# Kernel optimization log

Hardware: AMD Instinct MI355X
Metric: run time of the kernel (lower is better)

Reference implementation:

```python
import jax, jax.numpy as jnp
import numpy as np

N_INPUT, N_HIDDEN, N_OUTPUT = 64, 1024, 64
B, T = 128, 512

def setup_inputs() -> dict:
    key = jax.random.key(0)
    ks = jax.random.split(key, 8)
    s_in = 1.0 / np.sqrt(N_INPUT)
    s_h = 1.0 / np.sqrt(N_HIDDEN)
    return {
        "x": jax.random.normal(ks[0], (B, T, N_INPUT), jnp.float32),
        "enc_w": jax.random.uniform(ks[1], (N_HIDDEN, N_INPUT), jnp.float32, -s_in, s_in),
        "enc_b": jax.random.uniform(ks[2], (N_HIDDEN,), jnp.float32, -s_in, s_in),
        "rec_w": jax.random.uniform(ks[3], (N_HIDDEN, N_HIDDEN), jnp.float32, -s_h, s_h),
        "fgt_w": jax.random.uniform(ks[4], (N_HIDDEN, N_HIDDEN), jnp.float32, -s_h, s_h),
        "dec_w": jax.random.uniform(ks[5], (N_OUTPUT, N_HIDDEN), jnp.float32, -s_h, s_h),
        "dec_b": jax.random.uniform(ks[6], (N_OUTPUT,), jnp.float32, -s_h, s_h),
        "hinit_w": jax.random.uniform(ks[7], (N_HIDDEN, 1), jnp.float32, -1.0, 1.0),
        "hinit_b": jax.random.uniform(jax.random.fold_in(key, 9), (N_HIDDEN,), jnp.float32, -1.0, 1.0),
    }

def softsign(x):
    return x / (1.0 + jnp.abs(x))

def reference(x, enc_w, enc_b, rec_w, fgt_w, dec_w, dec_b, hinit_w, hinit_b):
    # x: [B, T, I] -> time-major [T, B, I]
    xt = jnp.transpose(x, (1, 0, 2))
    # hidden_init(ones(B,1)) = ones @ hinit_w^T + b = broadcast of column sum
    hidden0 = jnp.broadcast_to(hinit_w[:, 0] + hinit_b, (x.shape[0], hinit_b.shape[0]))
    # Precompute encoder projection for all timesteps (same math, one big GEMM)
    enc_all = jnp.einsum('tbi,hi->tbh', xt, enc_w) + enc_b  # [T, B, H]

    def step(hidden, enc_t):
        forget = jax.nn.sigmoid(hidden @ fgt_w.T)
        hidden_new = softsign(enc_t + hidden @ rec_w.T)
        hidden = (1.0 - forget) * hidden + forget * hidden_new
        out_t = hidden @ dec_w.T + dec_b
        return hidden, out_t

    hidden, output = jax.lax.scan(step, hidden0, enc_all)
    return output, hidden  # output: [T, B, O], hidden: [B, H]
```

## Files before the change

kernel.cpp:

```cpp
#include <hip/hip_runtime.h>

typedef unsigned short u16;

#define NWG 256
#define NT  256
#define TS  512
#define HD  1024
#define BS  128
#define NI  64
#define NO  64
#define XR  16
#define CC  32
#define RCP 17
#define MBW2 32

typedef __attribute__((ext_vector_type(8))) short bf16x8;
typedef __attribute__((ext_vector_type(4))) float f32x4;

__device__ __forceinline__ float bf2f(u16 u) {
    union { unsigned int i; float f; } v; v.i = ((unsigned int)u) << 16; return v.f;
}
__device__ __forceinline__ u16 f2bf(float f) {
    union { float fl; unsigned int i; } v; v.fl = f;
    unsigned int x = v.i;
    return (u16)((x + 0x7fffu + ((x >> 16) & 1u)) >> 16);
}
__device__ __forceinline__ float ldv(const void* p, size_t i, bool isf32) {
    return isf32 ? ((const float*)p)[i] : bf2f(((const u16*)p)[i]);
}

__device__ __forceinline__ unsigned l2_atomic_add(unsigned* p, unsigned v) {
    unsigned old;
    asm volatile("global_atomic_add %0, %1, %2, off sc0\n\t"
                 "s_waitcnt vmcnt(0)"
                 : "=&v"(old) : "v"(p), "v"(v) : "memory");
    return old;
}
__device__ __forceinline__ void l2_atomic_swap_nr(unsigned* p, unsigned v) {
    asm volatile("global_atomic_swap %0, %1, off" :: "v"(p), "v"(v) : "memory");
}

__device__ __forceinline__ void load_a_frags(const u16* ap, bf16x8* a) {
    asm volatile(
        "global_load_dwordx4 %0, %8, off sc0\n\t"
        "global_load_dwordx4 %1, %8, off offset:64 sc0\n\t"
        "global_load_dwordx4 %2, %8, off offset:128 sc0\n\t"
        "global_load_dwordx4 %3, %8, off offset:192 sc0\n\t"
        "global_load_dwordx4 %4, %8, off offset:256 sc0\n\t"
        "global_load_dwordx4 %5, %8, off offset:320 sc0\n\t"
        "global_load_dwordx4 %6, %8, off offset:384 sc0\n\t"
        "global_load_dwordx4 %7, %8, off offset:448 sc0\n\t"
        "s_waitcnt vmcnt(0)"
        : "=&v"(a[0]), "=&v"(a[1]), "=&v"(a[2]), "=&v"(a[3]),
          "=&v"(a[4]), "=&v"(a[5]), "=&v"(a[6]), "=&v"(a[7])
        : "v"(ap) : "memory");
}


__global__ __launch_bounds__(NT)
void arnn_xcd(const void* __restrict__ xv,
              const void* __restrict__ encwv,
              const void* __restrict__ encbv,
              const void* __restrict__ recwv,
              const void* __restrict__ fgtwv,
              const void* __restrict__ decwv,
              const void* __restrict__ decbv,
              const void* __restrict__ hinitwv,
              const void* __restrict__ hinitbv,
              void* __restrict__ outv,
              u16* __restrict__ h0buf,
              u16* __restrict__ h1buf,
              unsigned* __restrict__ tickets,
              unsigned* __restrict__ mboxes)
{
    __shared__ short WB[68 * 64 * 8];
    __shared__ float redC[2][4 * 5 * 16 * RCP];
    __shared__ unsigned s_xcd, s_slot;
    __shared__ int s_f32;

    const int tid  = threadIdx.x;
    const int wave = tid >> 6;
    const int lane = tid & 63;
    const int m    = lane & 15;
    const int quad = lane >> 4;

    if (tid == 0) {
        unsigned xcc;
        asm volatile("s_getreg_b32 %0, hwreg(HW_REG_XCC_ID, 0, 4)" : "=s"(xcc));
        xcc &= 7u;
        unsigned slot = l2_atomic_add(tickets + xcc * 16, 1u);
        s_xcd = xcc;
        s_slot = slot & 31u;
        s_f32 = 0;
    }
    __syncthreads();
    {
        float v = bf2f(((const u16*)recwv)[tid]);
        if (!(v >= -1.0f && v <= 1.0f)) s_f32 = 1;
    }
    __syncthreads();
    const bool isf32 = (s_f32 != 0);
    const int xcd  = (int)s_xcd;
    const int slot = (int)s_slot;
    const int b0   = xcd * XR;
    const int j0   = slot * CC;
    const int dt   = slot & 3;
    const int rg   = slot >> 2;
    unsigned* mbX = mboxes + (size_t)xcd * 32 * 4 * MBW2;
    unsigned* mbW = mbX + (slot * 4 + wave) * MBW2;
    const int pw = (slot >> 3), pi = (slot & 7);

    for (int idx = tid; idx < 68 * 64; idx += NT) {
        int ksg = idx >> 6, l = idx & 63, n = l & 15, q = l >> 4;
        int tile = (ksg < 34) ? 0 : 1;
        int ksl  = ksg - 34 * tile;
        int j = j0 + (tile << 4) + n;
        bf16x8 v;
        if (!isf32) {
            const u16* src = (ksl < 32) ? (const u16*)recwv + (size_t)j * HD + ksl * 32 + q * 8
                                        : (const u16*)encwv + (size_t)j * NI + (ksl - 32) * 32 + q * 8;
            v = *(const bf16x8*)src;
        } else {
            const float* src = (ksl < 32) ? (const float*)recwv + (size_t)j * HD + ksl * 32 + q * 8
                                          : (const float*)encwv + (size_t)j * NI + (ksl - 32) * 32 + q * 8;
            #pragma unroll
            for (int i = 0; i < 8; ++i) v[i] = (short)f2bf(src[i]);
        }
        *(bf16x8*)&WB[idx * 8] = v;
    }
    __syncthreads();

    bf16x8 Breg[2][8];
    #pragma unroll
    for (int ks = 0; ks < 8; ++ks) {
        int kb = wave * 8 + ks;
        Breg[0][ks] = *(const bf16x8*)&WB[((0  + kb) * 64 + lane) * 8];
        Breg[1][ks] = *(const bf16x8*)&WB[((34 + kb) * 64 + lane) * 8];
    }
    bf16x8 Ereg[2];
    if (wave < 2) {
        Ereg[0] = *(const bf16x8*)&WB[((32 + wave) * 64 + lane) * 8];
        Ereg[1] = *(const bf16x8*)&WB[((34 + 32 + wave) * 64 + lane) * 8];
    }
    __syncthreads();

    for (int idx = tid; idx < 64 * 64; idx += NT) {
        int ksg = idx >> 6, l = idx & 63, n = l & 15, q = l >> 4;
        int tile = ksg >> 5;
        int ksl  = ksg & 31;
        int j = j0 + (tile << 4) + n;
        bf16x8 v;
        if (!isf32) {
            v = *(const bf16x8*)((const u16*)fgtwv + (size_t)j * HD + ksl * 32 + q * 8);
        } else {
            const float* src = (const float*)fgtwv + (size_t)j * HD + ksl * 32 + q * 8;
            #pragma unroll
            for (int i = 0; i < 8; ++i) v[i] = (short)f2bf(src[i]);
        }
        *(bf16x8*)&WB[idx * 8] = v;
    }
    __syncthreads();

    bf16x8 Freg[2][8];
    #pragma unroll
    for (int ks = 0; ks < 8; ++ks) {
        int kb = wave * 8 + ks;
        Freg[0][ks] = *(const bf16x8*)&WB[((0  + kb) * 64 + lane) * 8];
        Freg[1][ks] = *(const bf16x8*)&WB[((32 + kb) * 64 + lane) * 8];
    }

    bf16x8 dfr[8];
    {
        int o = 16 * dt + m;
        #pragma unroll
        for (int ks = 0; ks < 8; ++ks) {
            int kb = wave * 256 + ks * 32 + quad * 8;
            if (!isf32) dfr[ks] = *(const bf16x8*)((const u16*)decwv + (size_t)o * HD + kb);
            else {
                const float* src = (const float*)decwv + (size_t)o * HD + kb;
                #pragma unroll
                for (int i = 0; i < 8; ++i) dfr[ks][i] = (short)f2bf(src[i]);
            }
        }
    }
    const int er2 = tid >> 4, ec2 = (tid & 15) * 2;
    float encb0 = ldv(encbv, j0 + ec2,     isf32);
    float encb1 = ldv(encbv, j0 + ec2 + 1, isf32);
    float decb_r = ldv(decbv, 16 * dt + (tid & 15), isf32);
    float hstA = ldv(hinitwv, j0 + ec2,     isf32) + ldv(hinitbv, j0 + ec2,     isf32);
    float hstB = ldv(hinitwv, j0 + ec2 + 1, isf32) + ldv(hinitbv, j0 + ec2 + 1, isf32);
    {
        unsigned pack = (unsigned)f2bf(hstA) | ((unsigned)f2bf(hstB) << 16);
        *(unsigned*)&h0buf[(size_t)(b0 + er2) * HD + j0 + ec2] = pack;
    }
    asm volatile("s_waitcnt vmcnt(0)" ::: "memory");
    if (lane < 32)
        l2_atomic_swap_nr(mbX + (lane * 4 + pw) * MBW2 + pi * 4 + wave, 1u);

    bf16x8 xpB = {};
    f32x4 xr0 = {}, xr1 = {};
    if (wave < 2) {
        size_t xb = (size_t)(b0 + m) * (TS * NI) + 0 * NI + wave * 32 + quad * 8;
        if (!isf32) xpB = *(const bf16x8*)((const u16*)xv + xb);
        else { const float* xp = (const float*)xv + xb;
               xr0 = *(const f32x4*)xp; xr1 = *(const f32x4*)(xp + 4); }
    }

    for (int t = 0; t < TS; ++t) {
        float* rc = redC[t & 1];
        f32x4 acc[5];
        #pragma unroll
        for (int tt = 0; tt < 5; ++tt) acc[tt] = (f32x4){0.f, 0.f, 0.f, 0.f};

        if (wave < 2) {
            bf16x8 xf;
            if (!isf32) xf = xpB;
            else {
                #pragma unroll
                for (int i = 0; i < 4; ++i) {
                    xf[i]     = (short)f2bf(xr0[i]);
                    xf[i + 4] = (short)f2bf(xr1[i]);
                }
            }
            acc[0] = __builtin_amdgcn_mfma_f32_16x16x32_bf16(xf, Ereg[0], acc[0], 0, 0, 0);
            acc[1] = __builtin_amdgcn_mfma_f32_16x16x32_bf16(xf, Ereg[1], acc[1], 0, 0, 0);
        }

        {
            const unsigned target = (unsigned)(t + 1);
            for (;;) {
                unsigned v = target;
                if (lane < 32) v = l2_atomic_add(mbW + lane, 0u);
                if (__all((int)(v >= target))) break;
            }
        }

        const u16* cur = (t & 1) ? h1buf : h0buf;
        u16*       nxt = (t & 1) ? h0buf : h1buf;

        bf16x8 a[8];
        load_a_frags(cur + (size_t)(b0 + m) * HD + wave * 256 + quad * 8, a);

        if (wave < 2) {
            int tn = (t + 1 < TS) ? t + 1 : t;
            size_t xb = (size_t)(b0 + m) * (TS * NI) + (size_t)tn * NI + wave * 32 + quad * 8;
            if (!isf32) xpB = *(const bf16x8*)((const u16*)xv + xb);
            else { const float* xp = (const float*)xv + xb;
                   xr0 = *(const f32x4*)xp; xr1 = *(const f32x4*)(xp + 4); }
        }

        #pragma unroll
        for (int ks = 0; ks < 8; ++ks) {
            acc[0] = __builtin_amdgcn_mfma_f32_16x16x32_bf16(a[ks], Breg[0][ks], acc[0], 0, 0, 0);
            acc[1] = __builtin_amdgcn_mfma_f32_16x16x32_bf16(a[ks], Breg[1][ks], acc[1], 0, 0, 0);
            acc[2] = __builtin_amdgcn_mfma_f32_16x16x32_bf16(a[ks], Freg[0][ks], acc[2], 0, 0, 0);
            acc[3] = __builtin_amdgcn_mfma_f32_16x16x32_bf16(a[ks], Freg[1][ks], acc[3], 0, 0, 0);
            acc[4] = __builtin_amdgcn_mfma_f32_16x16x32_bf16(a[ks], dfr[ks],     acc[4], 0, 0, 0);
        }

        #pragma unroll
        for (int tt = 0; tt < 5; ++tt) {
            #pragma unroll
            for (int r = 0; r < 4; ++r)
                rc[((wave * 5 + tt) * 16 + quad * 4 + r) * RCP + m] = acc[tt][r];
        }
        __syncthreads();

        {
            const int tl = ec2 >> 4, c0 = ec2 & 15;
            float pr0 = encb0, pf0 = 0.f, pr1 = encb1, pf1 = 0.f;
            #pragma unroll
            for (int kq = 0; kq < 4; ++kq) {
                pr0 += rc[((kq * 5 + tl) * 16 + er2) * RCP + c0];
                pf0 += rc[((kq * 5 + 2 + tl) * 16 + er2) * RCP + c0];
                pr1 += rc[((kq * 5 + tl) * 16 + er2) * RCP + c0 + 1];
                pf1 += rc[((kq * 5 + 2 + tl) * 16 + er2) * RCP + c0 + 1];
            }
            float fg0 = 1.0f / (1.0f + __expf(-pf0));
            float hn0 = pr0 / (1.0f + fabsf(pr0));
            hstA = hstA + fg0 * (hn0 - hstA);
            float fg1 = 1.0f / (1.0f + __expf(-pf1));
            float hn1 = pr1 / (1.0f + fabsf(pr1));
            hstB = hstB + fg1 * (hn1 - hstB);
            unsigned pack = (unsigned)f2bf(hstA) | ((unsigned)f2bf(hstB) << 16);
            *(unsigned*)&nxt[(size_t)(b0 + er2) * HD + j0 + ec2] = pack;
        }
        asm volatile("s_waitcnt vmcnt(0)" ::: "memory");
        if (lane < 32)
            l2_atomic_swap_nr(mbX + (lane * 4 + pw) * MBW2 + pi * 4 + wave, (unsigned)(t + 2));

        if (tid < 32 && t > 0) {
            int dr = 2 * rg + (tid >> 4), col = tid & 15;
            float o = decb_r;
            #pragma unroll
            for (int kq = 0; kq < 4; ++kq)
                o += rc[((kq * 5 + 4) * 16 + dr) * RCP + col];
            size_t oi = (size_t)(t - 1) * (BS * NO) + (size_t)(b0 + dr) * NO + 16 * dt + col;
            if (isf32) ((float*)outv)[oi] = o; else ((u16*)outv)[oi] = f2bf(o);
        }
    }

    {
        {
            const unsigned target = (unsigned)(TS + 1);
            for (;;) {
                unsigned v = target;
                if (lane < 32) v = l2_atomic_add(mbW + lane, 0u);
                if (__all((int)(v >= target))) break;
            }
        }
        float* rc = redC[0];
        bf16x8 a[8];
        load_a_frags(h0buf + (size_t)(b0 + m) * HD + wave * 256 + quad * 8, a);
        f32x4 ac = (f32x4){0.f, 0.f, 0.f, 0.f};
        #pragma unroll
        for (int ks = 0; ks < 8; ++ks)
            ac = __builtin_amdgcn_mfma_f32_16x16x32_bf16(a[ks], dfr[ks], ac, 0, 0, 0);
        #pragma unroll
        for (int r = 0; r < 4; ++r)
            rc[((wave * 5 + 4) * 16 + quad * 4 + r) * RCP + m] = ac[r];
        __syncthreads();
        if (tid < 32) {
            int dr = 2 * rg + (tid >> 4), col = tid & 15;
            float o = decb_r;
            #pragma unroll
            for (int kq = 0; kq < 4; ++kq)
                o += rc[((kq * 5 + 4) * 16 + dr) * RCP + col];
            size_t oi = (size_t)511 * (BS * NO) + (size_t)(b0 + dr) * NO + 16 * dt + col;
            if (isf32) ((float*)outv)[oi] = o; else ((u16*)outv)[oi] = f2bf(o);
        }
    }
    {
        size_t oi = (size_t)TS * BS * NO + (size_t)(b0 + er2) * HD + j0 + ec2;
        if (isf32) { ((float*)outv)[oi] = hstA; ((float*)outv)[oi + 1] = hstB; }
        else {
            unsigned pack = (unsigned)f2bf(hstA) | ((unsigned)f2bf(hstB) << 16);
            *(unsigned*)&((u16*)outv)[oi] = pack;
        }
    }
}

extern "C" void kernel_launch(void* const* d_in, const int* in_sizes, int n_in,
                              void* d_out, int out_size, void* d_ws, size_t ws_size,
                              hipStream_t stream) {
    (void)in_sizes; (void)n_in; (void)out_size; (void)ws_size;
    const void* xv       = d_in[0];
    const void* encwv    = d_in[1];
    const void* encbv    = d_in[2];
    const void* recwv    = d_in[3];
    const void* fgtwv    = d_in[4];
    const void* decwv    = d_in[5];
    const void* decbv    = d_in[6];
    const void* hinitwv  = d_in[7];
    const void* hinitbv  = d_in[8];
    void* outv = d_out;

    unsigned* tickets = (unsigned*)d_ws;
    unsigned* mboxes  = (unsigned*)((char*)d_ws + 4096);
    u16* h0buf = (u16*)((char*)d_ws + 524288);
    u16* h1buf = h0buf + (size_t)BS * HD;

    hipMemsetAsync(d_ws, 0, 4096 + 8 * 32 * 4 * MBW2 * 4, stream);

    void* args[] = { (void*)&xv, (void*)&encwv, (void*)&encbv, (void*)&recwv,
                     (void*)&fgtwv, (void*)&decwv, (void*)&decbv,
                     (void*)&hinitwv, (void*)&hinitbv,
                     (void*)&outv, (void*)&h0buf, (void*)&h1buf,
                     (void*)&tickets, (void*)&mboxes };
    hipError_t err = hipLaunchCooperativeKernel((void*)arnn_xcd, dim3(NWG), dim3(NT), args, 0, stream);
    if (err != hipSuccess) {
        hipLaunchKernelGGL(arnn_xcd, dim3(NWG), dim3(NT), 0, stream,
                           xv, encwv, encbv, recwv, fgtwv, decwv, decbv,
                           hinitwv, hinitbv, outv, h0buf, h1buf, tickets, mboxes);
    }
}
```

Measured before the change: 1.667 ms.

## Split each workgroup into two independent 8-row batch chains with per-chain barriers

Doubles the workgroup to 512 threads and splits it into two 4-wave chains, each handling 8 of the 16 batch rows with its own mailboxes, LDS reduction buffer and LDS spin barriers. The aim is to let one chain's MFMA and reduction work overlap the other chain's cross-workgroup wait on the recurrent dependency, and to poll fewer mailbox words. In exchange, half of each 16-row MFMA tile duplicates rows (m&7), register pressure and occupancy per CU change, and the custom LDS spin barriers add their own sync overhead.

```diff
diff --git a/kernel.cpp b/kernel.cpp
--- a/kernel.cpp
+++ b/kernel.cpp
@@ -3,16 +3,15 @@
 typedef unsigned short u16;
 
 #define NWG 256
-#define NT  256
+#define NT  512
 #define TS  512
 #define HD  1024
 #define BS  128
 #define NI  64
 #define NO  64
-#define XR  16
 #define CC  32
 #define RCP 17
-#define MBW2 32
+#define MBL 16
 
 typedef __attribute__((ext_vector_type(8))) short bf16x8;
 typedef __attribute__((ext_vector_type(4))) float f32x4;
@@ -75,12 +74,16 @@
 {
     __shared__ short WB[68 * 64 * 8];
     __shared__ float redC[2][4 * 5 * 16 * RCP];
+    __shared__ unsigned cbar[2][2];
     __shared__ unsigned s_xcd, s_slot;
     __shared__ int s_f32;
 
     const int tid  = threadIdx.x;
     const int wave = tid >> 6;
     const int lane = tid & 63;
+    const int chain= wave >> 2;
+    const int cw   = wave & 3;
+    const int ctid = tid & 255;
     const int m    = lane & 15;
     const int quad = lane >> 4;
 
@@ -93,6 +96,7 @@
         s_slot = slot & 31u;
         s_f32 = 0;
     }
+    if (tid < 4) ((unsigned*)cbar)[tid] = 0u;
     __syncthreads();
     {
         float v = bf2f(((const u16*)recwv)[tid]);
@@ -102,12 +106,11 @@
     const bool isf32 = (s_f32 != 0);
     const int xcd  = (int)s_xcd;
     const int slot = (int)s_slot;
-    const int b0   = xcd * XR;
+    const int b0c  = xcd * 16 + chain * 8;
     const int j0   = slot * CC;
     const int dt   = slot & 3;
-    const int rg   = slot >> 2;
-    unsigned* mbX = mboxes + (size_t)xcd * 32 * 4 * MBW2;
-    unsigned* mbW = mbX + (slot * 4 + wave) * MBW2;
+    unsigned* mbC = mboxes + ((size_t)(xcd * 2 + chain)) * 32 * 4 * MBL;
+    unsigned* mbW = mbC + (slot * 4 + cw) * MBL;
     const int pw = (slot >> 3), pi = (slot & 7);
 
     for (int idx = tid; idx < 68 * 64; idx += NT) {
@@ -129,21 +132,19 @@
         *(bf16x8*)&WB[idx * 8] = v;
     }
     __syncthreads();
-
     bf16x8 Breg[2][8];
     #pragma unroll
     for (int ks = 0; ks < 8; ++ks) {
-        int kb = wave * 8 + ks;
+        int kb = cw * 8 + ks;
         Breg[0][ks] = *(const bf16x8*)&WB[((0  + kb) * 64 + lane) * 8];
         Breg[1][ks] = *(const bf16x8*)&WB[((34 + kb) * 64 + lane) * 8];
     }
     bf16x8 Ereg[2];
-    if (wave < 2) {
-        Ereg[0] = *(const bf16x8*)&WB[((32 + wave) * 64 + lane) * 8];
-        Ereg[1] = *(const bf16x8*)&WB[((34 + 32 + wave) * 64 + lane) * 8];
-    }
-    __syncthreads();
-
+    if (cw < 2) {
+        Ereg[0] = *(const bf16x8*)&WB[((32 + cw) * 64 + lane) * 8];
+        Ereg[1] = *(const bf16x8*)&WB[((34 + 32 + cw) * 64 + lane) * 8];
+    }
+    __syncthreads();
     for (int idx = tid; idx < 64 * 64; idx += NT) {
         int ksg = idx >> 6, l = idx & 63, n = l & 15, q = l >> 4;
         int tile = ksg >> 5;
@@ -160,11 +161,10 @@
         *(bf16x8*)&WB[idx * 8] = v;
     }
     __syncthreads();
-
     bf16x8 Freg[2][8];
     #pragma unroll
     for (int ks = 0; ks < 8; ++ks) {
-        int kb = wave * 8 + ks;
+        int kb = cw * 8 + ks;
         Freg[0][ks] = *(const bf16x8*)&WB[((0  + kb) * 64 + lane) * 8];
         Freg[1][ks] = *(const bf16x8*)&WB[((32 + kb) * 64 + lane) * 8];
     }
@@ -174,7 +174,7 @@
         int o = 16 * dt + m;
         #pragma unroll
         for (int ks = 0; ks < 8; ++ks) {
-            int kb = wave * 256 + ks * 32 + quad * 8;
+            int kb = cw * 256 + ks * 32 + quad * 8;
             if (!isf32) dfr[ks] = *(const bf16x8*)((const u16*)decwv + (size_t)o * HD + kb);
             else {
                 const float* src = (const float*)decwv + (size_t)o * HD + kb;
@@ -183,36 +183,39 @@
             }
         }
     }
-    const int er2 = tid >> 4, ec2 = (tid & 15) * 2;
-    float encb0 = ldv(encbv, j0 + ec2,     isf32);
-    float encb1 = ldv(encbv, j0 + ec2 + 1, isf32);
-    float decb_r = ldv(decbv, 16 * dt + (tid & 15), isf32);
-    float hstA = ldv(hinitwv, j0 + ec2,     isf32) + ldv(hinitbv, j0 + ec2,     isf32);
-    float hstB = ldv(hinitwv, j0 + ec2 + 1, isf32) + ldv(hinitbv, j0 + ec2 + 1, isf32);
-    {
+    const int er = ctid >> 4, ec2 = (ctid & 15) * 2;
+    float encb0 = 0.f, encb1 = 0.f, hstA = 0.f, hstB = 0.f;
+    float decb_r = ldv(decbv, 16 * dt + (ctid & 15), isf32);
+    if (ctid < 128) {
+        encb0 = ldv(encbv, j0 + ec2,     isf32);
+        encb1 = ldv(encbv, j0 + ec2 + 1, isf32);
+        hstA = ldv(hinitwv, j0 + ec2,     isf32) + ldv(hinitbv, j0 + ec2,     isf32);
+        hstB = ldv(hinitwv, j0 + ec2 + 1, isf32) + ldv(hinitbv, j0 + ec2 + 1, isf32);
         unsigned pack = (unsigned)f2bf(hstA) | ((unsigned)f2bf(hstB) << 16);
-        *(unsigned*)&h0buf[(size_t)(b0 + er2) * HD + j0 + ec2] = pack;
-    }
-    asm volatile("s_waitcnt vmcnt(0)" ::: "memory");
-    if (lane < 32)
-        l2_atomic_swap_nr(mbX + (lane * 4 + pw) * MBW2 + pi * 4 + wave, 1u);
+        *(unsigned*)&h0buf[(size_t)(b0c + er) * HD + j0 + ec2] = pack;
+    }
+    __syncthreads();
+    if (cw == 0 && lane < 32)
+        l2_atomic_swap_nr(mbC + (lane * 4 + pw) * MBL + pi, 1u);
 
     bf16x8 xpB = {};
     f32x4 xr0 = {}, xr1 = {};
-    if (wave < 2) {
-        size_t xb = (size_t)(b0 + m) * (TS * NI) + 0 * NI + wave * 32 + quad * 8;
+    if (cw < 2) {
+        size_t xb = (size_t)(b0c + (m & 7)) * (TS * NI) + 0 * NI + cw * 32 + quad * 8;
         if (!isf32) xpB = *(const bf16x8*)((const u16*)xv + xb);
         else { const float* xp = (const float*)xv + xb;
                xr0 = *(const f32x4*)xp; xr1 = *(const f32x4*)(xp + 4); }
     }
 
+    float* rc = redC[chain];
+    volatile unsigned* vb1 = &cbar[chain][0];
+    volatile unsigned* vb2 = &cbar[chain][1];
     for (int t = 0; t < TS; ++t) {
-        float* rc = redC[t & 1];
         f32x4 acc[5];
         #pragma unroll
         for (int tt = 0; tt < 5; ++tt) acc[tt] = (f32x4){0.f, 0.f, 0.f, 0.f};
 
-        if (wave < 2) {
+        if (cw < 2) {
             bf16x8 xf;
             if (!isf32) xf = xpB;
             else {
@@ -230,7 +233,7 @@
             const unsigned target = (unsigned)(t + 1);
             for (;;) {
                 unsigned v = target;
-                if (lane < 32) v = l2_atomic_add(mbW + lane, 0u);
+                if (lane < 8) v = l2_atomic_add(mbW + lane, 0u);
                 if (__all((int)(v >= target))) break;
             }
         }
@@ -239,11 +242,11 @@
         u16*       nxt = (t & 1) ? h0buf : h1buf;
 
         bf16x8 a[8];
-        load_a_frags(cur + (size_t)(b0 + m) * HD + wave * 256 + quad * 8, a);
-
-        if (wave < 2) {
+        load_a_frags(cur + (size_t)(b0c + (m & 7)) * HD + cw * 256 + quad * 8, a);
+
+        if (cw < 2) {
             int tn = (t + 1 < TS) ? t + 1 : t;
-            size_t xb = (size_t)(b0 + m) * (TS * NI) + (size_t)tn * NI + wave * 32 + quad * 8;
+            size_t xb = (size_t)(b0c + (m & 7)) * (TS * NI) + (size_t)tn * NI + cw * 32 + quad * 8;
             if (!isf32) xpB = *(const bf16x8*)((const u16*)xv + xb);
             else { const float* xp = (const float*)xv + xb;
                    xr0 = *(const f32x4*)xp; xr1 = *(const f32x4*)(xp + 4); }
@@ -262,19 +265,24 @@
         for (int tt = 0; tt < 5; ++tt) {
             #pragma unroll
             for (int r = 0; r < 4; ++r)
-                rc[((wave * 5 + tt) * 16 + quad * 4 + r) * RCP + m] = acc[tt][r];
-        }
-        __syncthreads();
-
-        {
+                rc[((cw * 5 + tt) * 16 + quad * 4 + r) * RCP + m] = acc[tt][r];
+        }
+        asm volatile("s_waitcnt lgkmcnt(0)" ::: "memory");
+        if (lane == 0) atomicAdd((unsigned*)vb1, 1u);
+        {
+            const unsigned bt = 4u * (unsigned)(t + 1);
+            while (*vb1 < bt) {}
+        }
+
+        if (ctid < 128) {
             const int tl = ec2 >> 4, c0 = ec2 & 15;
             float pr0 = encb0, pf0 = 0.f, pr1 = encb1, pf1 = 0.f;
             #pragma unroll
             for (int kq = 0; kq < 4; ++kq) {
-                pr0 += rc[((kq * 5 + tl) * 16 + er2) * RCP + c0];
-                pf0 += rc[((kq * 5 + 2 + tl) * 16 + er2) * RCP + c0];
-                pr1 += rc[((kq * 5 + tl) * 16 + er2) * RCP + c0 + 1];
-                pf1 += rc[((kq * 5 + 2 + tl) * 16 + er2) * RCP + c0 + 1];
+                pr0 += rc[((kq * 5 + tl) * 16 + er) * RCP + c0];
+                pf0 += rc[((kq * 5 + 2 + tl) * 16 + er) * RCP + c0];
+                pr1 += rc[((kq * 5 + tl) * 16 + er) * RCP + c0 + 1];
+                pf1 += rc[((kq * 5 + 2 + tl) * 16 + er) * RCP + c0 + 1];
             }
             float fg0 = 1.0f / (1.0f + __expf(-pf0));
             float hn0 = pr0 / (1.0f + fabsf(pr0));
@@ -283,21 +291,25 @@
             float hn1 = pr1 / (1.0f + fabsf(pr1));
             hstB = hstB + fg1 * (hn1 - hstB);
             unsigned pack = (unsigned)f2bf(hstA) | ((unsigned)f2bf(hstB) << 16);
-            *(unsigned*)&nxt[(size_t)(b0 + er2) * HD + j0 + ec2] = pack;
+            *(unsigned*)&nxt[(size_t)(b0c + er) * HD + j0 + ec2] = pack;
+        }
+        if (slot < 4 && t > 0 && ctid < 128) {
+            int r = ctid >> 4, col = ctid & 15;
+            float o = decb_r;
+            #pragma unroll
+            for (int kq = 0; kq < 4; ++kq)
+                o += rc[((kq * 5 + 4) * 16 + r) * RCP + col];
+            size_t oi = (size_t)(t - 1) * (BS * NO) + (size_t)(b0c + r) * NO + 16 * dt + col;
+            if (isf32) ((float*)outv)[oi] = o; else ((u16*)outv)[oi] = f2bf(o);
         }
         asm volatile("s_waitcnt vmcnt(0)" ::: "memory");
-        if (lane < 32)
-            l2_atomic_swap_nr(mbX + (lane * 4 + pw) * MBW2 + pi * 4 + wave, (unsigned)(t + 2));
-
-        if (tid < 32 && t > 0) {
-            int dr = 2 * rg + (tid >> 4), col = tid & 15;
-            float o = decb_r;
-            #pragma unroll
-            for (int kq = 0; kq < 4; ++kq)
-                o += rc[((kq * 5 + 4) * 16 + dr) * RCP + col];
-            size_t oi = (size_t)(t - 1) * (BS * NO) + (size_t)(b0 + dr) * NO + 16 * dt + col;
-            if (isf32) ((float*)outv)[oi] = o; else ((u16*)outv)[oi] = f2bf(o);
-        }
+        if (lane == 0) atomicAdd((unsigned*)vb2, 1u);
+        {
+            const unsigned bt = 4u * (unsigned)(t + 1);
+            while (*vb2 < bt) {}
+        }
+        if (cw == 0 && lane < 32)
+            l2_atomic_swap_nr(mbC + (lane * 4 + pw) * MBL + pi, (unsigned)(t + 2));
     }
 
     {
@@ -305,33 +317,37 @@
             const unsigned target = (unsigned)(TS + 1);
             for (;;) {
                 unsigned v = target;
-                if (lane < 32) v = l2_atomic_add(mbW + lane, 0u);
+                if (lane < 8) v = l2_atomic_add(mbW + lane, 0u);
                 if (__all((int)(v >= target))) break;
             }
         }
-        float* rc = redC[0];
         bf16x8 a[8];
-        load_a_frags(h0buf + (size_t)(b0 + m) * HD + wave * 256 + quad * 8, a);
+        load_a_frags(h0buf + (size_t)(b0c + (m & 7)) * HD + cw * 256 + quad * 8, a);
         f32x4 ac = (f32x4){0.f, 0.f, 0.f, 0.f};
         #pragma unroll
         for (int ks = 0; ks < 8; ++ks)
             ac = __builtin_amdgcn_mfma_f32_16x16x32_bf16(a[ks], dfr[ks], ac, 0, 0, 0);
         #pragma unroll
         for (int r = 0; r < 4; ++r)
-            rc[((wave * 5 + 4) * 16 + quad * 4 + r) * RCP + m] = ac[r];
-        __syncthreads();
-        if (tid < 32) {
-            int dr = 2 * rg + (tid >> 4), col = tid & 15;
+            rc[((cw * 5 + 4) * 16 + quad * 4 + r) * RCP + m] = ac[r];
+        asm volatile("s_waitcnt lgkmcnt(0)" ::: "memory");
+        if (lane == 0) atomicAdd((unsigned*)vb1, 1u);
+        {
+            const unsigned bt = 4u * (unsigned)(TS + 1);
+            while (*vb1 < bt) {}
+        }
+        if (slot < 4 && ctid < 128) {
+            int r = ctid >> 4, col = ctid & 15;
             float o = decb_r;
             #pragma unroll
             for (int kq = 0; kq < 4; ++kq)
-                o += rc[((kq * 5 + 4) * 16 + dr) * RCP + col];
-            size_t oi = (size_t)511 * (BS * NO) + (size_t)(b0 + dr) * NO + 16 * dt + col;
+                o += rc[((kq * 5 + 4) * 16 + r) * RCP + col];
+            size_t oi = (size_t)511 * (BS * NO) + (size_t)(b0c + r) * NO + 16 * dt + col;
             if (isf32) ((float*)outv)[oi] = o; else ((u16*)outv)[oi] = f2bf(o);
         }
     }
-    {
-        size_t oi = (size_t)TS * BS * NO + (size_t)(b0 + er2) * HD + j0 + ec2;
+    if (ctid < 128) {
+        size_t oi = (size_t)TS * BS * NO + (size_t)(b0c + er) * HD + j0 + ec2;
         if (isf32) { ((float*)outv)[oi] = hstA; ((float*)outv)[oi + 1] = hstB; }
         else {
             unsigned pack = (unsigned)f2bf(hstA) | ((unsigned)f2bf(hstB) << 16);
@@ -360,7 +376,7 @@
     u16* h0buf = (u16*)((char*)d_ws + 524288);
     u16* h1buf = h0buf + (size_t)BS * HD;
 
-    hipMemsetAsync(d_ws, 0, 4096 + 8 * 32 * 4 * MBW2 * 4, stream);
+    hipMemsetAsync(d_ws, 0, 4096 + 8 * 2 * 32 * 4 * MBL * 4, stream);
 
     void* args[] = { (void*)&xv, (void*)&encwv, (void*)&encbv, (void*)&recwv,
                      (void*)&fgtwv, (void*)&decwv, (void*)&decbv,
```

New measurement: 2.397 ms. 1.44x slower.

## Split waves into K-halves × column tiles, cut reduction and mailbox traffic

Applied to the files above, without the earlier changes.

Work is now split across the four waves as two K-halves times two 16-column tiles, where before each wave took one K-quarter and covered every tile. The cross-wave reduction shrinks from a four-way LDS sum over five tiles to a two-way pairwise sum, and the gate update runs in MFMA accumulator layout in the kg==1 waves. Mailboxes drop from 4 per-wave flags to 2 per K-group, with a shared-memory counter so only the second finishing wave publishes, and decoder output is written only by the slots that own it. Each wave now loads 16 A fragments per step, which raises register pressure, and the hidden-state stores become scalar 16-bit writes.

```diff
diff --git a/kernel.cpp b/kernel.cpp
--- a/kernel.cpp
+++ b/kernel.cpp
@@ -11,8 +11,7 @@
 #define NO  64
 #define XR  16
 #define CC  32
-#define RCP 17
-#define MBW2 32
+#define MBL 16
 
 typedef __attribute__((ext_vector_type(8))) short bf16x8;
 typedef __attribute__((ext_vector_type(4))) float f32x4;
@@ -53,6 +52,31 @@
         "s_waitcnt vmcnt(0)"
         : "=&v"(a[0]), "=&v"(a[1]), "=&v"(a[2]), "=&v"(a[3]),
           "=&v"(a[4]), "=&v"(a[5]), "=&v"(a[6]), "=&v"(a[7])
+        : "v"(ap) : "memory");
+}
+__device__ __forceinline__ void load_a16(const u16* ap, bf16x8* a) {
+    asm volatile(
+        "global_load_dwordx4 %0, %16, off sc0\n\t"
+        "global_load_dwordx4 %1, %16, off offset:64 sc0\n\t"
+        "global_load_dwordx4 %2, %16, off offset:128 sc0\n\t"
+        "global_load_dwordx4 %3, %16, off offset:192 sc0\n\t"
+        "global_load_dwordx4 %4, %16, off offset:256 sc0\n\t"
+        "global_load_dwordx4 %5, %16, off offset:320 sc0\n\t"
+        "global_load_dwordx4 %6, %16, off offset:384 sc0\n\t"
+        "global_load_dwordx4 %7, %16, off offset:448 sc0\n\t"
+        "global_load_dwordx4 %8, %16, off offset:512 sc0\n\t"
+        "global_load_dwordx4 %9, %16, off offset:576 sc0\n\t"
+        "global_load_dwordx4 %10, %16, off offset:640 sc0\n\t"
+        "global_load_dwordx4 %11, %16, off offset:704 sc0\n\t"
+        "global_load_dwordx4 %12, %16, off offset:768 sc0\n\t"
+        "global_load_dwordx4 %13, %16, off offset:832 sc0\n\t"
+        "global_load_dwordx4 %14, %16, off offset:896 sc0\n\t"
+        "global_load_dwordx4 %15, %16, off offset:960 sc0\n\t"
+        "s_waitcnt vmcnt(0)"
+        : "=&v"(a[0]), "=&v"(a[1]), "=&v"(a[2]), "=&v"(a[3]),
+          "=&v"(a[4]), "=&v"(a[5]), "=&v"(a[6]), "=&v"(a[7]),
+          "=&v"(a[8]), "=&v"(a[9]), "=&v"(a[10]), "=&v"(a[11]),
+          "=&v"(a[12]), "=&v"(a[13]), "=&v"(a[14]), "=&v"(a[15])
         : "v"(ap) : "memory");
 }
 
@@ -74,13 +98,18 @@
               unsigned* __restrict__ mboxes)
 {
     __shared__ short WB[68 * 64 * 8];
-    __shared__ float redC[2][4 * 5 * 16 * RCP];
-    __shared__ unsigned s_xcd, s_slot;
+    __shared__ float recP[2][2][16][16];
+    __shared__ float fgtP[2][2][16][16];
+    __shared__ float decP[2][4][16][16];
+    __shared__ float decbS[16];
+    __shared__ unsigned s_xcd, s_slot, jc;
     __shared__ int s_f32;
 
     const int tid  = threadIdx.x;
     const int wave = tid >> 6;
     const int lane = tid & 63;
+    const int kg   = wave >> 1;
+    const int cg   = wave & 1;
     const int m    = lane & 15;
     const int quad = lane >> 4;
 
@@ -92,6 +121,7 @@
         s_xcd = xcc;
         s_slot = slot & 31u;
         s_f32 = 0;
+        jc = 0u;
     }
     __syncthreads();
     {
@@ -105,10 +135,9 @@
     const int b0   = xcd * XR;
     const int j0   = slot * CC;
     const int dt   = slot & 3;
-    const int rg   = slot >> 2;
-    unsigned* mbX = mboxes + (size_t)xcd * 32 * 4 * MBW2;
-    unsigned* mbW = mbX + (slot * 4 + wave) * MBW2;
-    const int pw = (slot >> 3), pi = (slot & 7);
+    unsigned* mbX = mboxes + (size_t)xcd * 32 * 2 * MBL;
+    unsigned* mbW = mbX + (slot * 2 + kg) * MBL;
+    const int pg = slot >> 4, pi = slot & 15;
 
     for (int idx = tid; idx < 68 * 64; idx += NT) {
         int ksg = idx >> 6, l = idx & 63, n = l & 15, q = l >> 4;
@@ -129,25 +158,19 @@
         *(bf16x8*)&WB[idx * 8] = v;
     }
     __syncthreads();
-
-    bf16x8 Breg[2][8];
+    bf16x8 Breg[16];
     #pragma unroll
-    for (int ks = 0; ks < 8; ++ks) {
-        int kb = wave * 8 + ks;
-        Breg[0][ks] = *(const bf16x8*)&WB[((0  + kb) * 64 + lane) * 8];
-        Breg[1][ks] = *(const bf16x8*)&WB[((34 + kb) * 64 + lane) * 8];
-    }
-    bf16x8 Ereg[2];
-    if (wave < 2) {
-        Ereg[0] = *(const bf16x8*)&WB[((32 + wave) * 64 + lane) * 8];
-        Ereg[1] = *(const bf16x8*)&WB[((34 + 32 + wave) * 64 + lane) * 8];
-    }
-    __syncthreads();
-
+    for (int ks = 0; ks < 16; ++ks)
+        Breg[ks] = *(const bf16x8*)&WB[((cg * 34 + kg * 16 + ks) * 64 + lane) * 8];
+    bf16x8 Ereg[2] = {};
+    if (kg == 0) {
+        Ereg[0] = *(const bf16x8*)&WB[((cg * 34 + 32) * 64 + lane) * 8];
+        Ereg[1] = *(const bf16x8*)&WB[((cg * 34 + 33) * 64 + lane) * 8];
+    }
+    __syncthreads();
     for (int idx = tid; idx < 64 * 64; idx += NT) {
         int ksg = idx >> 6, l = idx & 63, n = l & 15, q = l >> 4;
-        int tile = ksg >> 5;
-        int ksl  = ksg & 31;
+        int tile = ksg >> 5, ksl = ksg & 31;
         int j = j0 + (tile << 4) + n;
         bf16x8 v;
         if (!isf32) {
@@ -160,21 +183,18 @@
         *(bf16x8*)&WB[idx * 8] = v;
     }
     __syncthreads();
-
-    bf16x8 Freg[2][8];
+    bf16x8 Freg[16];
     #pragma unroll
-    for (int ks = 0; ks < 8; ++ks) {
-        int kb = wave * 8 + ks;
-        Freg[0][ks] = *(const bf16x8*)&WB[((0  + kb) * 64 + lane) * 8];
-        Freg[1][ks] = *(const bf16x8*)&WB[((32 + kb) * 64 + lane) * 8];
-    }
+    for (int ks = 0; ks < 16; ++ks)
+        Freg[ks] = *(const bf16x8*)&WB[((cg * 32 + kg * 16 + ks) * 64 + lane) * 8];
 
     bf16x8 dfr[8];
     {
         int o = 16 * dt + m;
+        int kqb = kg * 512 + cg * 256;
         #pragma unroll
         for (int ks = 0; ks < 8; ++ks) {
-            int kb = wave * 256 + ks * 32 + quad * 8;
+            int kb = kqb + ks * 32 + quad * 8;
             if (!isf32) dfr[ks] = *(const bf16x8*)((const u16*)decwv + (size_t)o * HD + kb);
             else {
                 const float* src = (const float*)decwv + (size_t)o * HD + kb;
@@ -183,54 +203,63 @@
             }
         }
     }
-    const int er2 = tid >> 4, ec2 = (tid & 15) * 2;
-    float encb0 = ldv(encbv, j0 + ec2,     isf32);
-    float encb1 = ldv(encbv, j0 + ec2 + 1, isf32);
-    float decb_r = ldv(decbv, 16 * dt + (tid & 15), isf32);
-    float hstA = ldv(hinitwv, j0 + ec2,     isf32) + ldv(hinitbv, j0 + ec2,     isf32);
-    float hstB = ldv(hinitwv, j0 + ec2 + 1, isf32) + ldv(hinitbv, j0 + ec2 + 1, isf32);
-    {
-        unsigned pack = (unsigned)f2bf(hstA) | ((unsigned)f2bf(hstB) << 16);
-        *(unsigned*)&h0buf[(size_t)(b0 + er2) * HD + j0 + ec2] = pack;
-    }
-    asm volatile("s_waitcnt vmcnt(0)" ::: "memory");
-    if (lane < 32)
-        l2_atomic_swap_nr(mbX + (lane * 4 + pw) * MBW2 + pi * 4 + wave, 1u);
-
-    bf16x8 xpB = {};
-    f32x4 xr0 = {}, xr1 = {};
-    if (wave < 2) {
-        size_t xb = (size_t)(b0 + m) * (TS * NI) + 0 * NI + wave * 32 + quad * 8;
-        if (!isf32) xpB = *(const bf16x8*)((const u16*)xv + xb);
-        else { const float* xp = (const float*)xv + xb;
-               xr0 = *(const f32x4*)xp; xr1 = *(const f32x4*)(xp + 4); }
+    if (tid < 16) decbS[tid] = ldv(decbv, 16 * dt + tid, isf32);
+
+    const int mycol = j0 + cg * 16 + m;
+    float encb_r = 0.f;
+    float hst[4] = {0.f, 0.f, 0.f, 0.f};
+    if (kg == 1) {
+        encb_r = ldv(encbv, mycol, isf32);
+        float h0v = ldv(hinitwv, mycol, isf32) + ldv(hinitbv, mycol, isf32);
+        #pragma unroll
+        for (int r = 0; r < 4; ++r) {
+            hst[r] = h0v;
+            h0buf[(size_t)(b0 + quad * 4 + r) * HD + mycol] = f2bf(h0v);
+        }
+    }
+    __syncthreads();
+    if (tid < 32)
+        l2_atomic_swap_nr(mbX + (tid * 2 + pg) * MBL + pi, 1u);
+
+    bf16x8 xp0 = {}, xp1 = {};
+    f32x4 xr0 = {}, xr1 = {}, xr2 = {}, xr3 = {};
+    if (kg == 0) {
+        size_t xb = (size_t)(b0 + m) * (TS * NI) + 0 * NI + quad * 8;
+        if (!isf32) {
+            xp0 = *(const bf16x8*)((const u16*)xv + xb);
+            xp1 = *(const bf16x8*)((const u16*)xv + xb + 32);
+        } else {
+            const float* xp = (const float*)xv + xb;
+            xr0 = *(const f32x4*)xp;        xr1 = *(const f32x4*)(xp + 4);
+            xr2 = *(const f32x4*)(xp + 32); xr3 = *(const f32x4*)(xp + 36);
+        }
     }
 
     for (int t = 0; t < TS; ++t) {
-        float* rc = redC[t & 1];
-        f32x4 acc[5];
-        #pragma unroll
-        for (int tt = 0; tt < 5; ++tt) acc[tt] = (f32x4){0.f, 0.f, 0.f, 0.f};
-
-        if (wave < 2) {
-            bf16x8 xf;
-            if (!isf32) xf = xpB;
+        const int pp = t & 1;
+        f32x4 acc0 = (f32x4){0.f, 0.f, 0.f, 0.f};
+        f32x4 acc1 = (f32x4){0.f, 0.f, 0.f, 0.f};
+        f32x4 dacc = (f32x4){0.f, 0.f, 0.f, 0.f};
+
+        if (kg == 0) {
+            bf16x8 xf0, xf1;
+            if (!isf32) { xf0 = xp0; xf1 = xp1; }
             else {
                 #pragma unroll
                 for (int i = 0; i < 4; ++i) {
-                    xf[i]     = (short)f2bf(xr0[i]);
-                    xf[i + 4] = (short)f2bf(xr1[i]);
+                    xf0[i] = (short)f2bf(xr0[i]); xf0[i + 4] = (short)f2bf(xr1[i]);
+                    xf1[i] = (short)f2bf(xr2[i]); xf1[i + 4] = (short)f2bf(xr3[i]);
                 }
             }
-            acc[0] = __builtin_amdgcn_mfma_f32_16x16x32_bf16(xf, Ereg[0], acc[0], 0, 0, 0);
-            acc[1] = __builtin_amdgcn_mfma_f32_16x16x32_bf16(xf, Ereg[1], acc[1], 0, 0, 0);
+            acc0 = __builtin_amdgcn_mfma_f32_16x16x32_bf16(xf0, Ereg[0], acc0, 0, 0, 0);
+            acc0 = __builtin_amdgcn_mfma_f32_16x16x32_bf16(xf1, Ereg[1], acc0, 0, 0, 0);
         }
 
         {
             const unsigned target = (unsigned)(t + 1);
             for (;;) {
                 unsigned v = target;
-                if (lane < 32) v = l2_atomic_add(mbW + lane, 0u);
+                if (lane < 16) v = l2_atomic_add(mbW + lane, 0u);
                 if (__all((int)(v >= target))) break;
             }
         }
@@ -238,65 +267,80 @@
         const u16* cur = (t & 1) ? h1buf : h0buf;
         u16*       nxt = (t & 1) ? h0buf : h1buf;
 
-        bf16x8 a[8];
-        load_a_frags(cur + (size_t)(b0 + m) * HD + wave * 256 + quad * 8, a);
-
-        if (wave < 2) {
+        bf16x8 a[16];
+        load_a16(cur + (size_t)(b0 + m) * HD + kg * 512 + quad * 8, a);
+
+        if (kg == 0) {
             int tn = (t + 1 < TS) ? t + 1 : t;
-            size_t xb = (size_t)(b0 + m) * (TS * NI) + (size_t)tn * NI + wave * 32 + quad * 8;
-            if (!isf32) xpB = *(const bf16x8*)((const u16*)xv + xb);
-            else { const float* xp = (const float*)xv + xb;
-                   xr0 = *(const f32x4*)xp; xr1 = *(const f32x4*)(xp + 4); }
+            size_t xb = (size_t)(b0 + m) * (TS * NI) + (size_t)tn * NI + quad * 8;
+            if (!isf32) {
+                xp0 = *(const bf16x8*)((const u16*)xv + xb);
+                xp1 = *(const bf16x8*)((const u16*)xv + xb + 32);
+            } else {
+                const float* xp = (const float*)xv + xb;
+                xr0 = *(const f32x4*)xp;        xr1 = *(const f32x4*)(xp + 4);
+                xr2 = *(const f32x4*)(xp + 32); xr3 = *(const f32x4*)(xp + 36);
+            }
         }
 
         #pragma unroll
-        for (int ks = 0; ks < 8; ++ks) {
-            acc[0] = __builtin_amdgcn_mfma_f32_16x16x32_bf16(a[ks], Breg[0][ks], acc[0], 0, 0, 0);
-            acc[1] = __builtin_amdgcn_mfma_f32_16x16x32_bf16(a[ks], Breg[1][ks], acc[1], 0, 0, 0);
-            acc[2] = __builtin_amdgcn_mfma_f32_16x16x32_bf16(a[ks], Freg[0][ks], acc[2], 0, 0, 0);
-            acc[3] = __builtin_amdgcn_mfma_f32_16x16x32_bf16(a[ks], Freg[1][ks], acc[3], 0, 0, 0);
-            acc[4] = __builtin_amdgcn_mfma_f32_16x16x32_bf16(a[ks], dfr[ks],     acc[4], 0, 0, 0);
-        }
-
-        #pragma unroll
-        for (int tt = 0; tt < 5; ++tt) {
+        for (int ks = 0; ks < 16; ++ks) {
+            acc0 = __builtin_amdgcn_mfma_f32_16x16x32_bf16(a[ks], Breg[ks], acc0, 0, 0, 0);
+            acc1 = __builtin_amdgcn_mfma_f32_16x16x32_bf16(a[ks], Freg[ks], acc1, 0, 0, 0);
+        }
+        if (cg == 0) {
+            #pragma unroll
+            for (int ks = 0; ks < 8; ++ks)
+                dacc = __builtin_amdgcn_mfma_f32_16x16x32_bf16(a[ks], dfr[ks], dacc, 0, 0, 0);
+        } else {
+            #pragma unroll
+            for (int ks = 0; ks < 8; ++ks)
+                dacc = __builtin_amdgcn_mfma_f32_16x16x32_bf16(a[8 + ks], dfr[ks], dacc, 0, 0, 0);
+        }
+
+        if (kg == 0) {
+            #pragma unroll
+            for (int r = 0; r < 4; ++r) {
+                recP[pp][cg][quad * 4 + r][m] = acc0[r];
+                fgtP[pp][cg][quad * 4 + r][m] = acc1[r];
+            }
+        }
+        {
+            const int kq = kg * 2 + cg;
             #pragma unroll
             for (int r = 0; r < 4; ++r)
-                rc[((wave * 5 + tt) * 16 + quad * 4 + r) * RCP + m] = acc[tt][r];
+                decP[pp][kq][quad * 4 + r][m] = dacc[r];
         }
         __syncthreads();
 
-        {
-            const int tl = ec2 >> 4, c0 = ec2 & 15;
-            float pr0 = encb0, pf0 = 0.f, pr1 = encb1, pf1 = 0.f;
-            #pragma unroll
-            for (int kq = 0; kq < 4; ++kq) {
-                pr0 += rc[((kq * 5 + tl) * 16 + er2) * RCP + c0];
-                pf0 += rc[((kq * 5 + 2 + tl) * 16 + er2) * RCP + c0];
-                pr1 += rc[((kq * 5 + tl) * 16 + er2) * RCP + c0 + 1];
-                pf1 += rc[((kq * 5 + 2 + tl) * 16 + er2) * RCP + c0 + 1];
-            }
-            float fg0 = 1.0f / (1.0f + __expf(-pf0));
-            float hn0 = pr0 / (1.0f + fabsf(pr0));
-            hstA = hstA + fg0 * (hn0 - hstA);
-            float fg1 = 1.0f / (1.0f + __expf(-pf1));
-            float hn1 = pr1 / (1.0f + fabsf(pr1));
-            hstB = hstB + fg1 * (hn1 - hstB);
-            unsigned pack = (unsigned)f2bf(hstA) | ((unsigned)f2bf(hstB) << 16);
-            *(unsigned*)&nxt[(size_t)(b0 + er2) * HD + j0 + ec2] = pack;
-        }
-        asm volatile("s_waitcnt vmcnt(0)" ::: "memory");
-        if (lane < 32)
-            l2_atomic_swap_nr(mbX + (lane * 4 + pw) * MBW2 + pi * 4 + wave, (unsigned)(t + 2));
-
-        if (tid < 32 && t > 0) {
-            int dr = 2 * rg + (tid >> 4), col = tid & 15;
-            float o = decb_r;
-            #pragma unroll
-            for (int kq = 0; kq < 4; ++kq)
-                o += rc[((kq * 5 + 4) * 16 + dr) * RCP + col];
-            size_t oi = (size_t)(t - 1) * (BS * NO) + (size_t)(b0 + dr) * NO + 16 * dt + col;
-            if (isf32) ((float*)outv)[oi] = o; else ((u16*)outv)[oi] = f2bf(o);
+        if (kg == 1) {
+            #pragma unroll
+            for (int r = 0; r < 4; ++r) {
+                int row = quad * 4 + r;
+                float pr = acc0[r] + recP[pp][cg][row][m] + encb_r;
+                float pf = acc1[r] + fgtP[pp][cg][row][m];
+                float fg = 1.0f / (1.0f + __expf(-pf));
+                float hn = pr / (1.0f + fabsf(pr));
+                hst[r] = hst[r] + fg * (hn - hst[r]);
+                nxt[(size_t)(b0 + row) * HD + mycol] = f2bf(hst[r]);
+            }
+            asm volatile("s_waitcnt vmcnt(0)" ::: "memory");
+            int old = 0;
+            if (lane == 0) old = (int)atomicAdd(&jc, 1u);
+            old = __shfl(old, 0);
+            if (old == 2 * t + 1 && lane < 32)
+                l2_atomic_swap_nr(mbX + (lane * 2 + pg) * MBL + pi, (unsigned)(t + 2));
+            if (slot < 4 && cg == 0 && t > 0) {
+                #pragma unroll
+                for (int e = 0; e < 4; ++e) {
+                    int idx = lane * 4 + e, row = idx >> 4, col = idx & 15;
+                    float o = decbS[col];
+                    #pragma unroll
+                    for (int kq = 0; kq < 4; ++kq) o += decP[pp][kq][row][col];
+                    size_t oi = (size_t)(t - 1) * (BS * NO) + (size_t)(b0 + row) * NO + 16 * dt + col;
+                    if (isf32) ((float*)outv)[oi] = o; else ((u16*)outv)[oi] = f2bf(o);
+                }
+            }
         }
     }
 
@@ -305,37 +349,38 @@
             const unsigned target = (unsigned)(TS + 1);
             for (;;) {
                 unsigned v = target;
-                if (lane < 32) v = l2_atomic_add(mbW + lane, 0u);
+                if (lane < 16) v = l2_atomic_add(mbW + lane, 0u);
                 if (__all((int)(v >= target))) break;
             }
         }
-        float* rc = redC[0];
-        bf16x8 a[8];
-        load_a_frags(h0buf + (size_t)(b0 + m) * HD + wave * 256 + quad * 8, a);
-        f32x4 ac = (f32x4){0.f, 0.f, 0.f, 0.f};
+        bf16x8 ad[8];
+        load_a_frags(h0buf + (size_t)(b0 + m) * HD + kg * 512 + cg * 256 + quad * 8, ad);
+        f32x4 dc = (f32x4){0.f, 0.f, 0.f, 0.f};
         #pragma unroll
         for (int ks = 0; ks < 8; ++ks)
-            ac = __builtin_amdgcn_mfma_f32_16x16x32_bf16(a[ks], dfr[ks], ac, 0, 0, 0);
+            dc = __builtin_amdgcn_mfma_f32_16x16x32_bf16(ad[ks], dfr[ks], dc, 0, 0, 0);
+        const int kq = kg * 2 + cg;
         #pragma unroll
         for (int r = 0; r < 4; ++r)
-            rc[((wave * 5 + 4) * 16 + quad * 4 + r) * RCP + m] = ac[r];
+            decP[0][kq][quad * 4 + r][m] = dc[r];
         __syncthreads();
-        if (tid < 32) {
-            int dr = 2 * rg + (tid >> 4), col = tid & 15;
-            float o = decb_r;
-            #pragma unroll
-            for (int kq = 0; kq < 4; ++kq)
-                o += rc[((kq * 5 + 4) * 16 + dr) * RCP + col];
-            size_t oi = (size_t)511 * (BS * NO) + (size_t)(b0 + dr) * NO + 16 * dt + col;
-            if (isf32) ((float*)outv)[oi] = o; else ((u16*)outv)[oi] = f2bf(o);
-        }
-    }
-    {
-        size_t oi = (size_t)TS * BS * NO + (size_t)(b0 + er2) * HD + j0 + ec2;
-        if (isf32) { ((float*)outv)[oi] = hstA; ((float*)outv)[oi + 1] = hstB; }
-        else {
-            unsigned pack = (unsigned)f2bf(hstA) | ((unsigned)f2bf(hstB) << 16);
-            *(unsigned*)&((u16*)outv)[oi] = pack;
+        if (slot < 4 && wave == 2) {
+            #pragma unroll
+            for (int e = 0; e < 4; ++e) {
+                int idx = lane * 4 + e, row = idx >> 4, col = idx & 15;
+                float o = decbS[col];
+                #pragma unroll
+                for (int kqq = 0; kqq < 4; ++kqq) o += decP[0][kqq][row][col];
+                size_t oi = (size_t)511 * (BS * NO) + (size_t)(b0 + row) * NO + 16 * dt + col;
+                if (isf32) ((float*)outv)[oi] = o; else ((u16*)outv)[oi] = f2bf(o);
+            }
+        }
+        if (kg == 1) {
+            #pragma unroll
+            for (int r = 0; r < 4; ++r) {
+                size_t oi = (size_t)TS * BS * NO + (size_t)(b0 + quad * 4 + r) * HD + mycol;
+                if (isf32) ((float*)outv)[oi] = hst[r]; else ((u16*)outv)[oi] = f2bf(hst[r]);
+            }
         }
     }
 }
@@ -360,7 +405,7 @@
     u16* h0buf = (u16*)((char*)d_ws + 524288);
     u16* h1buf = h0buf + (size_t)BS * HD;
 
-    hipMemsetAsync(d_ws, 0, 4096 + 8 * 32 * 4 * MBW2 * 4, stream);
+    hipMemsetAsync(d_ws, 0, 4096 + 8 * 32 * 2 * MBL * 4, stream);
 
     void* args[] = { (void*)&xv, (void*)&encwv, (void*)&encbv, (void*)&recwv,
                      (void*)&fgtwv, (void*)&decwv, (void*)&decbv,
```

After: 2.125 ms. +27.5%, slower.
